# Kernel optimization log

Hardware: AMD Instinct MI355X
Metric: run time of the kernel (lower is better)

Reference implementation:

```python
import jax, jax.numpy as jnp
import numpy as np

B, J, C = 4096, 17, 512       # batch, joints (length), channels (dim)
K, TOK, CH, H, KS, G = 3, 64, 1024, 8, 3, 8  # adj kernels, tokens_dim, channels_dim, heads, conv_large, gn groups
EPS = 1e-5


def setup_inputs() -> dict:
    key = jax.random.key(0)
    ks = jax.random.split(key, 16)
    r = lambda i, shp, s=0.02: jax.random.normal(ks[i], shp, jnp.float32) * s
    return {
        "x": jax.random.normal(ks[0], (B, J, C), jnp.float32),
        "adj": jax.random.uniform(ks[1], (K, J, J), jnp.float32) / J,
        "norm1_w": jnp.ones((J,), jnp.float32), "norm1_b": jnp.zeros((J,), jnp.float32),
        "gcn1_w": r(2, (K * C, C)), "gcn1_b": jnp.zeros((K * C,), jnp.float32),
        "dw_w": r(3, (C, 1, KS), 0.1), "dw_b": jnp.zeros((C,), jnp.float32),
        "gn1_w": jnp.ones((C,), jnp.float32), "gn1_b": jnp.zeros((C,), jnp.float32),
        "pw_w": r(4, (C, C)), "pw_b": jnp.zeros((C,), jnp.float32),
        "mlp1_w1": r(5, (TOK, J)), "mlp1_b1": jnp.zeros((TOK,), jnp.float32),
        "mlp1_w2": r(6, (J, TOK)), "mlp1_b2": jnp.zeros((J,), jnp.float32),
        "qkv_w": r(7, (3 * C, C)), "qkv_b": jnp.zeros((3 * C,), jnp.float32),
        "proj_w": r(8, (C, C)), "proj_b": jnp.zeros((C,), jnp.float32),
        "gnf_w": jnp.ones((C,), jnp.float32), "gnf_b": jnp.zeros((C,), jnp.float32),
        "norm2_w": jnp.ones((C,), jnp.float32), "norm2_b": jnp.zeros((C,), jnp.float32),
        "mlp2_w1": r(9, (CH, C)), "mlp2_b1": jnp.zeros((CH,), jnp.float32),
        "mlp2_w2": r(10, (C, CH)), "mlp2_b2": jnp.zeros((C,), jnp.float32),
        "gcn2_w": r(11, (K * C, C)), "gcn2_b": jnp.zeros((K * C,), jnp.float32),
    }


def _gelu(t):
    return jax.nn.gelu(t, approximate=False)  # torch nn.GELU default is exact erf


def _ln(t, w, b):  # LayerNorm over last axis
    m = t.mean(-1, keepdims=True)
    v = ((t - m) ** 2).mean(-1, keepdims=True)
    return (t - m) * jax.lax.rsqrt(v + EPS) * w + b


def _gn(t, w, b):  # GroupNorm(G, C) over (B, C, J)
    Bn, Cc, Jn = t.shape
    r = t.reshape(Bn, G, -1)
    m = r.mean(-1, keepdims=True)
    v = ((r - m) ** 2).mean(-1, keepdims=True)
    r = (r - m) * jax.lax.rsqrt(v + EPS)
    return r.reshape(Bn, Cc, Jn) * w[:, None] + b[:, None]


def _gcn(t, w, b, adj):  # t: (B,C,J); 1x1 conv to K*C then einsum with adj (K,J,J)
    y = jnp.einsum('bcj,oc->boj', t, w) + b[:, None]
    y = y.reshape(t.shape[0], K, C, t.shape[2])
    return jnp.einsum('bkcv,kvw->bcw', y, adj)


def reference(x, adj, norm1_w, norm1_b, gcn1_w, gcn1_b, dw_w, dw_b, gn1_w, gn1_b,
              pw_w, pw_b, mlp1_w1, mlp1_b1, mlp1_w2, mlp1_b2, qkv_w, qkv_b,
              proj_w, proj_b, gnf_w, gnf_b, norm2_w, norm2_b,
              mlp2_w1, mlp2_b1, mlp2_w2, mlp2_b2, gcn2_w, gcn2_b):
    res = x                                   # (B,J,C)
    xc = jnp.swapaxes(x, 1, 2)                # (B,C,J)
    xc = _ln(xc, norm1_w, norm1_b)            # LayerNorm over joints

    # --- branch 1: GCN ---
    x_gcn1 = _gcn(xc, gcn1_w, gcn1_b, adj)    # (B,C,J)

    # --- branch 2: depthwise conv + token MLP ---
    h = jax.lax.conv_general_dilated(xc, dw_w, (1,), [(KS // 2, KS // 2)],
                                     dimension_numbers=('NCH', 'OIH', 'NCH'),
                                     feature_group_count=C) + dw_b[:, None]
    h = _gelu(_gn(h, gn1_w, gn1_b))
    h = jnp.einsum('bcj,oc->boj', h, pw_w) + pw_b[:, None]      # 1x1 conv
    h = _gelu(jnp.einsum('bcj,tj->bct', h, mlp1_w1) + mlp1_b1)  # token mlp fc1
    h = jnp.einsum('bct,jt->bcj', h, mlp1_w2) + mlp1_b2         # token mlp fc2

    # --- branch 3: global spatial attention over joints ---
    dh = C // H
    qkv = jnp.einsum('bcj,oc->boj', xc, qkv_w) + qkv_b[:, None]  # (B,3C,J)
    q, k_, v_ = jnp.split(qkv, 3, axis=1)
    q = q.reshape(-1, H, dh, J); k_ = k_.reshape(-1, H, dh, J); v_ = v_.reshape(-1, H, dh, J)
    attn = jax.nn.softmax(jnp.einsum('bhdi,bhdj->bhij', q, k_) / jnp.sqrt(jnp.float32(dh)), axis=-1)
    sga = jnp.einsum('bhij,bhdj->bhdi', attn, v_).reshape(-1, C, J)
    sga = jnp.einsum('bcj,oc->boj', sga, proj_w) + proj_b[:, None]

    # --- fuse ---
    xc = _gelu(_gn(sga + x_gcn1 + h, gnf_w, gnf_b))
    xj = jnp.swapaxes(xc, 1, 2)               # (B,J,C)
    res_channel = xj
    xn = _ln(xj + res, norm2_w, norm2_b)      # LayerNorm over channels
    m = _gelu(jnp.einsum('bjc,hc->bjh', xn, mlp2_w1) + mlp2_b1)
    m = jnp.einsum('bjh,ch->bjc', m, mlp2_w2) + mlp2_b2
    g2 = _gcn(jnp.swapaxes(m, 1, 2), gcn2_w, gcn2_b, adj)  # (B,C,J)
    xj = res_channel + jnp.swapaxes(g2, 1, 2)
    return xj + res
```

## Files before the change

kernel.cpp:

```cpp
#include <hip/hip_runtime.h>
#include <stdint.h>

#define BB 4096
#define JJ 17
#define CC 512

typedef unsigned short u16;
typedef __bf16 bf16x8 __attribute__((ext_vector_type(8)));
typedef float  f32x4  __attribute__((ext_vector_type(4)));

__device__ __forceinline__ float bf2f(u16 u){ return __uint_as_float(((uint32_t)u)<<16); }
__device__ __forceinline__ u16 f2bf(float f){
  uint32_t u = __float_as_uint(f);
  u += 0x7fffu + ((u>>16)&1u);
  return (u16)(u>>16);
}
__device__ __forceinline__ void unpk2(uint32_t u, float& lo, float& hi){
  lo = __uint_as_float(u<<16);
  hi = __uint_as_float(u & 0xffff0000u);
}
__device__ __forceinline__ float gelu_f(float x){
  float x2 = x*x;
  float y2 = x*fmaf(0.0713548162726f, x2, 1.59576912161f);
  float ey = __builtin_amdgcn_exp2f(y2*1.44269504089f);
  return fmaf(-x, __builtin_amdgcn_rcpf(ey+1.f), x);
}
__device__ __forceinline__ void gll16(const void* g, void* l){
  __builtin_amdgcn_global_load_lds(
      (const __attribute__((address_space(1))) void*)g,
      (__attribute__((address_space(3))) void*)l, 16, 0, 0);
}

__global__ void k_cvt7(const float* __restrict__ s0,const float* __restrict__ s1,
                       const float* __restrict__ s2,const float* __restrict__ s3,
                       const float* __restrict__ s4,const float* __restrict__ s5,
                       const float* __restrict__ s6, u16* __restrict__ out){
  int i = blockIdx.x*blockDim.x + threadIdx.x;
  if (i >= 3932160) return;
  const float* src; int off;
  if      (i < 786432)  { src=s0; off=0; }
  else if (i < 1572864) { src=s1; off=786432; }
  else if (i < 1835008) { src=s2; off=1572864; }
  else if (i < 2097152) { src=s3; off=1835008; }
  else if (i < 2621440) { src=s4; off=2097152; }
  else if (i < 3145728) { src=s5; off=2621440; }
  else                  { src=s6; off=3145728; }
  out[i] = f2bf(src[i-off]);
}

__global__ void k_tokprep(const float* __restrict__ w1, const float* __restrict__ w2,
                          u16* __restrict__ w1m, u16* __restrict__ w2m){
  int i = blockIdx.x*blockDim.x + threadIdx.x;
  if (i < 2560){ int t=i/40, j=i%40; w1m[i] = (j<17) ? f2bf(w1[t*17+j]) : (u16)0; }
  int k = i - 2560;
  if (k >= 0 && k < 2304){ int j=k/72, t=k%72; w2m[k] = (j<17 && t<64) ? f2bf(w2[j*64+t]) : (u16)0; }
}

__global__ __launch_bounds__(512) void k_pre(
    const float* __restrict__ x, int b0,
    const float* __restrict__ n1w, const float* __restrict__ n1b,
    const float* __restrict__ dww, const float* __restrict__ dwb,
    const float* __restrict__ gn1w, const float* __restrict__ gn1b,
    u16* __restrict__ xc, u16* __restrict__ hgn)
{
  int b = blockIdx.x, c = threadIdx.x;
  const float* xp = x + (size_t)(b0+b)*JJ*CC + c;
  float v[JJ]; float s = 0.f;
  #pragma unroll
  for (int j=0;j<JJ;j++){ v[j] = xp[(size_t)j*CC]; s += v[j]; }
  float mn = s*(1.f/JJ); float var = 0.f;
  #pragma unroll
  for (int j=0;j<JJ;j++){ float d=v[j]-mn; var += d*d; }
  float rr = rsqrtf(var*(1.f/JJ)+1e-5f);
  float xcv[JJ];
  #pragma unroll
  for (int j=0;j<JJ;j++) xcv[j] = (v[j]-mn)*rr*n1w[j] + n1b[j];
  u16* xo = xc + (size_t)b*JJ*CC + c;
  #pragma unroll
  for (int j=0;j<JJ;j++) xo[(size_t)j*CC] = f2bf(xcv[j]);
  float w0=dww[c*3+0], w1=dww[c*3+1], w2=dww[c*3+2], db=dwb[c];
  float h[JJ];
  #pragma unroll
  for (int j=0;j<JJ;j++){
    float a = db + w1*xcv[j];
    if (j>0)    a += w0*xcv[j-1];
    if (j<JJ-1) a += w2*xcv[j+1];
    h[j] = a;
  }
  float ss=0.f, sq=0.f;
  #pragma unroll
  for (int j=0;j<JJ;j++){ ss += h[j]; sq += h[j]*h[j]; }
  for (int off=32; off; off>>=1){ ss += __shfl_xor(ss,off); sq += __shfl_xor(sq,off); }
  float gm = ss*(1.f/(64.f*JJ));
  float gr = rsqrtf(sq*(1.f/(64.f*JJ)) - gm*gm + 1e-5f);
  float gw = gn1w[c], gb = gn1b[c];
  u16* ho = hgn + (size_t)b*JJ*CC + c;
  #pragma unroll
  for (int j=0;j<JJ;j++){
    float t = (h[j]-gm)*gr*gw + gb;
    ho[(size_t)j*CC] = f2bf(gelu_f(t));
  }
}

template<int DO_GELU, int DO_ADD>
__global__ __launch_bounds__(512,4) void gemm_r5(
    const u16* __restrict__ A, const u16* __restrict__ W, const float* __restrict__ bias,
    u16* __restrict__ out, const u16* __restrict__ add0, const u16* __restrict__ add1,
    int M, int N, int K, int NXT)
{
  __shared__ __align__(16) u16 lds[36864];
  const int tid = threadIdx.x;
  const int wid = tid>>6, lane = tid&63;

  const int nwg = gridDim.x;
  const int q8 = nwg>>3, r8 = nwg&7;
  const int xcd = blockIdx.x & 7, sub = blockIdx.x >> 3;
  const int wg = (xcd<r8 ? xcd*(q8+1) : r8*(q8+1)+(xcd-r8)*q8) + sub;
  const int n0 = (wg % NXT)*256;
  const int m0 = (wg / NXT)*128;

  const int wm = wid>>2, wn = wid&3;
  const int lr = lane&15, lg = lane>>4;
  const int T  = K>>5;

  const int agsw = ((tid&3) ^ ((tid>>3)&3))<<3;
  const u16* gA  = A + (size_t)(m0 + (tid>>2))*K + agsw;
  const u16* gB0 = W + (size_t)(n0 + (tid>>2))*K + agsw;
  const u16* gB1 = W + (size_t)(n0 + 128 + (tid>>2))*K + agsw;
  const int dstl = tid*8;

  const int g8 = (lg ^ ((lr>>1)&3))<<3;
  const int offA0 = (wm*64+lr)*32 + g8;
  const int offB0 = 4096 + (wn*64+lr)*32 + g8;

  f32x4 acc[4][4];
  #pragma unroll
  for (int i=0;i<4;i++)
    #pragma unroll
    for (int j=0;j<4;j++) acc[i][j] = (f32x4){0.f,0.f,0.f,0.f};

  auto STAGE = [&](int t, int sofs){
    gll16(gA  + t*32, lds + sofs + dstl);
    gll16(gB0 + t*32, lds + sofs + 4096 + dstl);
    gll16(gB1 + t*32, lds + sofs + 8192 + dstl);
  };

  STAGE(0, 0); STAGE(1, 12288);
  asm volatile("s_waitcnt vmcnt(3)" ::: "memory");
  __builtin_amdgcn_s_barrier();

  int s0 = 0, s1 = 12288, s2 = 24576;
  for (int t=0; t<T; ++t){
    const bool more = (t+2 < T);
    if (more) STAGE(t+2, s2);
    bf16x8 av[4], bv[4];
    #pragma unroll
    for (int i=0;i<4;i++) av[i] = *(const bf16x8*)&lds[s0 + offA0 + i*512];
    #pragma unroll
    for (int j=0;j<4;j++) bv[j] = *(const bf16x8*)&lds[s0 + offB0 + j*512];
    __builtin_amdgcn_s_setprio(1);
    #pragma unroll
    for (int i=0;i<4;i++)
      #pragma unroll
      for (int j=0;j<4;j++)
        acc[i][j] = __builtin_amdgcn_mfma_f32_16x16x32_bf16(av[i], bv[j], acc[i][j], 0,0,0);
    __builtin_amdgcn_s_setprio(0);
    if (more) asm volatile("s_waitcnt vmcnt(3)" ::: "memory");
    else      asm volatile("s_waitcnt vmcnt(0)" ::: "memory");
    __builtin_amdgcn_s_barrier();
    const int tmp = s0; s0 = s1; s1 = s2; s2 = tmp;
  }

  const int rbase = lg*4;
  #pragma unroll
  for (int i=0;i<4;i++){
    #pragma unroll
    for (int j=0;j<4;j++){
      const int col  = n0 + wn*64 + j*16 + lr;
      const int row0 = m0 + wm*64 + i*16 + rbase;
      const float bvl = bias[col];
      #pragma unroll
      for (int r=0;r<4;r++){
        size_t idx = (size_t)(row0+r)*N + col;
        float v = acc[i][j][r] + bvl;
        if (DO_ADD)  v += bf2f(add0[idx]) + bf2f(add1[idx]);
        if (DO_GELU) v = gelu_f(v);
        out[idx] = f2bf(v);
      }
    }
  }
}

template<int FINAL>
__global__ __launch_bounds__(512) void k_gcn2(
    const u16* __restrict__ G, const float* __restrict__ adj,
    u16* __restrict__ xg,
    const u16* __restrict__ tsum, int b0,
    float* __restrict__ out)
{
  __shared__ __align__(16) float adjp[51*20];
  const int tid = threadIdx.x;
  for (int i=tid; i<1020; i+=512){
    int r=i/20, cl=i%20;
    adjp[i] = (cl<17) ? adj[r*17+cl] : 0.f;
  }
  __syncthreads();

  const int sl  = tid>>7;
  const int l   = tid&127;
  const int c0  = l*4;
  const int bl  = blockIdx.x*4 + sl;

  float acc[JJ][4];
  #pragma unroll
  for (int w=0;w<JJ;w++)
    #pragma unroll
    for (int e=0;e<4;e++) acc[w][e]=0.f;

  const u16* gbase = G + (size_t)bl*JJ*1536 + c0;
  #pragma unroll 3
  for (int kv=0; kv<51; kv++){
    const int k = kv/JJ, v = kv - k*JJ;
    uint2 yu = *(const uint2*)(gbase + (size_t)v*1536 + k*512);
    float y0,y1,y2,y3;
    unpk2(yu.x, y0, y1);
    unpk2(yu.y, y2, y3);
    const f32x4* arow = (const f32x4*)&adjp[kv*20];
    f32x4 a0=arow[0], a1=arow[1], a2=arow[2], a3=arow[3];
    float a16 = adjp[kv*20+16];
    float ar[JJ] = {a0[0],a0[1],a0[2],a0[3], a1[0],a1[1],a1[2],a1[3],
                    a2[0],a2[1],a2[2],a2[3], a3[0],a3[1],a3[2],a3[3], a16};
    #pragma unroll
    for (int w=0;w<JJ;w++){
      acc[w][0] += y0*ar[w];
      acc[w][1] += y1*ar[w];
      acc[w][2] += y2*ar[w];
      acc[w][3] += y3*ar[w];
    }
  }

  if (FINAL==0){
    u16* xo = xg + (size_t)bl*JJ*CC + c0;
    #pragma unroll
    for (int w=0;w<JJ;w++){
      uint2 o;
      o.x = (uint32_t)f2bf(acc[w][0]) | ((uint32_t)f2bf(acc[w][1])<<16);
      o.y = (uint32_t)f2bf(acc[w][2]) | ((uint32_t)f2bf(acc[w][3])<<16);
      *(uint2*)(xo + (size_t)w*CC) = o;
    }
  } else {
    const size_t lb = (size_t)bl*JJ*CC + c0;
    const size_t gb = (size_t)(b0+bl)*JJ*CC + c0;
    #pragma unroll
    for (int w=0;w<JJ;w++){
      uint2 tu = *(const uint2*)(tsum + lb + (size_t)w*CC);
      float t0,t1,t2,t3;
      unpk2(tu.x, t0, t1);
      unpk2(tu.y, t2, t3);
      f32x4 o;
      o[0]=acc[w][0]+t0; o[1]=acc[w][1]+t1;
      o[2]=acc[w][2]+t2; o[3]=acc[w][3]+t3;
      *(f32x4*)(out + gb + (size_t)w*CC) = o;
    }
  }
}

__global__ __launch_bounds__(512) void k_attn(const u16* __restrict__ Gqkv, u16* __restrict__ sga){
  __shared__ __align__(16) u16 qs[8*17*72];
  __shared__ __align__(16) u16 ks_[8*17*72];
  __shared__ __align__(16) float at[8*17*20];
  int b = blockIdx.x, tid = threadIdx.x;
  int h = tid>>6, d = tid&63;
  const u16* base = Gqkv + (size_t)b*JJ*1536;
  float vv[JJ];
  #pragma unroll
  for (int i=0;i<JJ;i++){
    qs [(h*JJ+i)*72 + d] = base[(size_t)i*1536 +        h*64 + d];
    ks_[(h*JJ+i)*72 + d] = base[(size_t)i*1536 +  512 + h*64 + d];
    vv[i] = bf2f(base[(size_t)i*1536 + 1024 + h*64 + d]);
  }
  __syncthreads();
  for (int p=d; p<289; p+=64){
    int i=p/JJ, j=p-i*JJ;
    const u16* qrow = &qs [(h*JJ+i)*72];
    const u16* krow = &ks_[(h*JJ+j)*72];
    float a=0.f;
    #pragma unroll
    for (int t=0;t<8;t++){
      bf16x8 q8 = *(const bf16x8*)&qrow[t*8];
      bf16x8 k8 = *(const bf16x8*)&krow[t*8];
      #pragma unroll
      for (int e=0;e<8;e++) a += (float)q8[e]*(float)k8[e];
    }
    at[(h*JJ+i)*20 + j] = a*0.125f;
  }
  __syncthreads();
  if (d < JJ){
    float* row = &at[(h*JJ+d)*20];
    f32x4 r0=((f32x4*)row)[0], r1=((f32x4*)row)[1], r2=((f32x4*)row)[2], r3=((f32x4*)row)[3];
    float e16=row[16];
    float rv[JJ]={r0[0],r0[1],r0[2],r0[3],r1[0],r1[1],r1[2],r1[3],
                  r2[0],r2[1],r2[2],r2[3],r3[0],r3[1],r3[2],r3[3],e16};
    float mx=-1e30f;
    #pragma unroll
    for (int j=0;j<JJ;j++) mx=fmaxf(mx,rv[j]);
    float sm=0.f;
    #pragma unroll
    for (int j=0;j<JJ;j++){ rv[j]=__builtin_amdgcn_exp2f((rv[j]-mx)*1.44269504089f); sm+=rv[j]; }
    float inv=1.f/sm;
    #pragma unroll
    for (int j=0;j<JJ;j++) row[j]=rv[j]*inv;
  }
  __syncthreads();
  #pragma unroll
  for (int i=0;i<JJ;i++){
    const float* row = &at[(h*JJ+i)*20];
    f32x4 r0=((const f32x4*)row)[0], r1=((const f32x4*)row)[1],
          r2=((const f32x4*)row)[2], r3=((const f32x4*)row)[3];
    float a = r0[0]*vv[0]+r0[1]*vv[1]+r0[2]*vv[2]+r0[3]*vv[3]
            + r1[0]*vv[4]+r1[1]*vv[5]+r1[2]*vv[6]+r1[3]*vv[7]
            + r2[0]*vv[8]+r2[1]*vv[9]+r2[2]*vv[10]+r2[3]*vv[11]
            + r3[0]*vv[12]+r3[1]*vv[13]+r3[2]*vv[14]+r3[3]*vv[15]
            + row[16]*vv[16];
    sga[((size_t)b*JJ+i)*CC + h*64 + d] = f2bf(a);
  }
}

__global__ __launch_bounds__(256) void k_tok(const u16* __restrict__ Hpw,
    const u16* __restrict__ w1m, const u16* __restrict__ w2m,
    const float* __restrict__ b1, const float* __restrict__ b2,
    u16* __restrict__ h2o){
  __shared__ __align__(16) u16 lds[31488];
  __shared__ float b1s[64], b2s[32];
  const int tid = threadIdx.x, wid = tid>>6, lane = tid&63;
  const int lr = lane&15, lg = lane>>4;
  const int bl = blockIdx.x;
  const f32x4 zz = {0.f,0.f,0.f,0.f};

  for (int i=tid; i<2560; i+=256) lds[26624+i] = w1m[i];
  for (int i=tid; i<2304; i+=256) lds[29184+i] = w2m[i];
  if (tid<64) b1s[tid] = b1[tid];
  if (tid<32) b2s[tid] = (tid<17) ? b2[tid] : 0.f;
  {
    const int base = tid*40;
    lds[base+17]=0; lds[base+18]=0; lds[base+19]=0;
    #pragma unroll
    for (int q=0;q<5;q++) *(uint2*)&lds[base+20+q*4] = (uint2){0u,0u};
  }
  __syncthreads();

  const u16* hp = Hpw + (size_t)bl*JJ*CC;
  u16* op = h2o + (size_t)bl*JJ*CC;

  for (int pass=0; pass<2; ++pass){
    const int cbase = pass*256;
    for (int idx=tid; idx<1088; idx+=256){
      int j = idx>>6, cq = (idx&63)<<2;
      uint2 u = *(const uint2*)(hp + (size_t)j*CC + cbase + cq);
      lds[(cq  )*40 + j] = (u16)(u.x & 0xffffu);
      lds[(cq+1)*40 + j] = (u16)(u.x >> 16);
      lds[(cq+2)*40 + j] = (u16)(u.y & 0xffffu);
      lds[(cq+3)*40 + j] = (u16)(u.y >> 16);
    }
    __syncthreads();

    bf16x8 av1[4];
    #pragma unroll
    for (int mt=0;mt<4;mt++) av1[mt] = *(const bf16x8*)&lds[26624 + (mt*16+lr)*40 + lg*8];
    #pragma unroll
    for (int nt=0;nt<4;nt++){
      const int cl = wid*64 + nt*16 + lr;
      bf16x8 bv = *(const bf16x8*)&lds[cl*40 + lg*8];
      #pragma unroll
      for (int mt=0;mt<4;mt++){
        f32x4 ac = __builtin_amdgcn_mfma_f32_16x16x32_bf16(av1[mt], bv, zz, 0,0,0);
        const int t0 = mt*16 + lg*4;
        float g0 = gelu_f(ac[0] + b1s[t0+0]);
        float g1 = gelu_f(ac[1] + b1s[t0+1]);
        float g2 = gelu_f(ac[2] + b1s[t0+2]);
        float g3 = gelu_f(ac[3] + b1s[t0+3]);
        uint2 pk;
        pk.x = (uint32_t)f2bf(g0) | ((uint32_t)f2bf(g1)<<16);
        pk.y = (uint32_t)f2bf(g2) | ((uint32_t)f2bf(g3)<<16);
        const int gi = (10240 + cl*64 + t0) ^ ((cl&7)<<3);
        *(uint2*)&lds[gi] = pk;
      }
    }
    asm volatile("s_waitcnt lgkmcnt(0)" ::: "memory");
    __builtin_amdgcn_sched_barrier(0);

    bf16x8 av2[2][2];
    #pragma unroll
    for (int mt=0;mt<2;mt++)
      #pragma unroll
      for (int kt=0;kt<2;kt++)
        av2[mt][kt] = *(const bf16x8*)&lds[29184 + (mt*16+lr)*72 + kt*32 + lg*8];
    #pragma unroll
    for (int nt=0;nt<4;nt++){
      const int cl = wid*64 + nt*16 + lr;
      f32x4 a20 = zz, a21 = zz;
      #pragma unroll
      for (int kt=0;kt<2;kt++){
        const int gi = (10240 + cl*64 + kt*32 + lg*8) ^ ((cl&7)<<3);
        bf16x8 bv2 = *(const bf16x8*)&lds[gi];
        a20 = __builtin_amdgcn_mfma_f32_16x16x32_bf16(av2[0][kt], bv2, a20, 0,0,0);
        a21 = __builtin_amdgcn_mfma_f32_16x16x32_bf16(av2[1][kt], bv2, a21, 0,0,0);
      }
      const int c = cbase + cl;
      #pragma unroll
      for (int r=0;r<4;r++){
        const int j = lg*4 + r;
        op[(size_t)j*CC + c] = f2bf(a20[r] + b2s[j]);
      }
      if (lg==0) op[(size_t)16*CC + c] = f2bf(a21[0] + b2s[16]);
    }
    __syncthreads();
  }
}

__global__ __launch_bounds__(512) void k_fuse(const u16* __restrict__ s,
    const float* __restrict__ x, int b0,
    const float* __restrict__ gfw, const float* __restrict__ gfb,
    const float* __restrict__ n2w, const float* __restrict__ n2b,
    u16* __restrict__ tsum, u16* __restrict__ xn){
  __shared__ float rS[8][JJ], rQ[8][JJ];
  int b = blockIdx.x, c = threadIdx.x;
  int wave = c>>6, lane = c&63;
  const u16* sp = s + (size_t)b*JJ*CC + c;
  float sv[JJ];
  #pragma unroll
  for (int j=0;j<JJ;j++) sv[j]=bf2f(sp[(size_t)j*CC]);
  float ss=0.f, sq=0.f;
  #pragma unroll
  for (int j=0;j<JJ;j++){ ss+=sv[j]; sq+=sv[j]*sv[j]; }
  for (int off=32; off; off>>=1){ ss += __shfl_xor(ss,off); sq += __shfl_xor(sq,off); }
  float gm = ss*(1.f/1088.f);
  float gr = rsqrtf(sq*(1.f/1088.f) - gm*gm + 1e-5f);
  float gw=gfw[c], gb=gfb[c];
  const float* xp = x + (size_t)(b0+b)*JJ*CC + c;
  u16* tp = tsum + (size_t)b*JJ*CC + c;
  float t[JJ];
  #pragma unroll
  for (int j=0;j<JJ;j++){
    float v = gelu_f((sv[j]-gm)*gr*gw + gb);
    t[j] = v + xp[(size_t)j*CC];
    tp[(size_t)j*CC] = f2bf(t[j]);
  }
  #pragma unroll
  for (int j=0;j<JJ;j++){
    float a=t[j], q=a*a;
    for (int off=32; off; off>>=1){ a+=__shfl_xor(a,off); q+=__shfl_xor(q,off); }
    if (lane==0){ rS[wave][j]=a; rQ[wave][j]=q; }
  }
  __syncthreads();
  float wN=n2w[c], bN=n2b[c];
  u16* xo = xn + (size_t)b*JJ*CC + c;
  #pragma unroll
  for (int j=0;j<JJ;j++){
    float S=0.f,Q=0.f;
    #pragma unroll
    for (int w=0;w<8;w++){ S+=rS[w][j]; Q+=rQ[w][j]; }
    float mn=S*(1.f/512.f);
    float r2=rsqrtf(Q*(1.f/512.f)-mn*mn+1e-5f);
    xo[(size_t)j*CC]=f2bf((t[j]-mn)*r2*wN+bN);
  }
}

extern "C" void kernel_launch(void* const* d_in, const int* in_sizes, int n_in,
                              void* d_out, int out_size, void* d_ws, size_t ws_size,
                              hipStream_t stream)
{
  const float* x      = (const float*)d_in[0];
  const float* adj    = (const float*)d_in[1];
  const float* n1w    = (const float*)d_in[2];
  const float* n1b    = (const float*)d_in[3];
  const float* gcn1_w = (const float*)d_in[4];
  const float* gcn1_b = (const float*)d_in[5];
  const float* dw_w   = (const float*)d_in[6];
  const float* dw_b   = (const float*)d_in[7];
  const float* gn1_w  = (const float*)d_in[8];
  const float* gn1_b  = (const float*)d_in[9];
  const float* pw_w   = (const float*)d_in[10];
  const float* pw_b   = (const float*)d_in[11];
  const float* m1w1   = (const float*)d_in[12];
  const float* m1b1   = (const float*)d_in[13];
  const float* m1w2   = (const float*)d_in[14];
  const float* m1b2   = (const float*)d_in[15];
  const float* qkv_w  = (const float*)d_in[16];
  const float* qkv_b  = (const float*)d_in[17];
  const float* proj_w = (const float*)d_in[18];
  const float* proj_b = (const float*)d_in[19];
  const float* gnf_w  = (const float*)d_in[20];
  const float* gnf_b  = (const float*)d_in[21];
  const float* n2w    = (const float*)d_in[22];
  const float* n2b    = (const float*)d_in[23];
  const float* m2w1   = (const float*)d_in[24];
  const float* m2b1   = (const float*)d_in[25];
  const float* m2w2   = (const float*)d_in[26];
  const float* m2b2   = (const float*)d_in[27];
  const float* gcn2_w = (const float*)d_in[28];
  const float* gcn2_b = (const float*)d_in[29];
  float* out = (float*)d_out;

  char* ws = (char*)d_ws;
  const size_t WBYTES = (size_t)3932160*2;
  const size_t TPBYTES = (2560+2304)*2;

  const int cands[5] = {4096,2048,1024,512,256};
  int NB = 0;
  for (int ci=0; ci<5; ci++){
    size_t need = WBYTES + TPBYTES + (size_t)cands[ci]*JJ*2*(1536 + 4*512);
    if (need <= ws_size){ NB = cands[ci]; break; }
  }
  if (NB == 0) return;

  u16* wb = (u16*)ws;
  u16* w1m = (u16*)(ws + WBYTES);
  u16* w2m = w1m + 2560;
  char* p = ws + WBYTES + TPBYTES;
  const size_t SZ_BIGc = (size_t)NB*JJ*1536*2;
  const size_t SZTc    = (size_t)NB*JJ*512*2;
  u16* big = (u16*)p;               p += SZ_BIGc;
  u16* t0  = (u16*)p;               p += SZTc;
  u16* t1  = (u16*)p;               p += SZTc;
  u16* t2  = (u16*)p;               p += SZTc;
  u16* t3  = (u16*)p;

  u16 *wg1=wb, *wqkv=wb+786432, *wpw=wb+1572864, *wproj=wb+1835008,
      *wm1=wb+2097152, *wm2=wb+2621440, *wg2=wb+3145728;

  k_cvt7<<<(3932160+255)/256,256,0,stream>>>(gcn1_w,qkv_w,pw_w,proj_w,m2w1,m2w2,gcn2_w,wb);
  k_tokprep<<<19,256,0,stream>>>(m1w1,m1w2,w1m,w2m);

  const int M2 = NB*JJ;
  const int MT = M2/128;
  for (int b0 = 0; b0 < BB; b0 += NB){
    k_pre<<<NB,512,0,stream>>>(x,b0,n1w,n1b,dw_w,dw_b,gn1_w,gn1_b, t0, t1);
    gemm_r5<0,0><<<MT*6,512,0,stream>>>(t0,wg1,gcn1_b,big,nullptr,nullptr,M2,1536,512,6);
    k_gcn2<0><<<NB/4,512,0,stream>>>(big,adj,t2,nullptr,0,nullptr);
    gemm_r5<0,0><<<MT*6,512,0,stream>>>(t0,wqkv,qkv_b,big,nullptr,nullptr,M2,1536,512,6);
    k_attn<<<NB,512,0,stream>>>(big,t3);
    gemm_r5<0,0><<<MT*2,512,0,stream>>>(t1,wpw,pw_b,t0,nullptr,nullptr,M2,512,512,2);
    k_tok<<<NB,256,0,stream>>>(t0,w1m,w2m,m1b1,m1b2,t1);
    gemm_r5<0,1><<<MT*2,512,0,stream>>>(t3,wproj,proj_b,t0,t2,t1,M2,512,512,2);
    k_fuse<<<NB,512,0,stream>>>(t0,x,b0,gnf_w,gnf_b,n2w,n2b,t3,t2);
    gemm_r5<1,0><<<MT*4,512,0,stream>>>(t2,wm1,m2b1,big,nullptr,nullptr,M2,1024,512,4);
    gemm_r5<0,0><<<MT*2,512,0,stream>>>(big,wm2,m2b2,t0,nullptr,nullptr,M2,512,1024,2);
    gemm_r5<0,0><<<MT*6,512,0,stream>>>(t0,wg2,gcn2_b,big,nullptr,nullptr,M2,1536,512,6);
    k_gcn2<1><<<NB/4,512,0,stream>>>(big,adj,nullptr,t3,b0,out);
  }
}
```

Measured before the change: 1.329 ms.

## Enlarge GEMM tile to 256x256 with split-phase A/B staging

The shared bf16 GEMM used for all the linear layers now computes a 256x256 output tile per workgroup instead of 128x256. Each wave accumulates 8x4 MFMA tiles, and each K-step runs in two halves: the A loads for the next stage are issued before the first half and the B loads before the second, with an extra barrier in between. The aim is to reuse the B fragments across twice as many rows and to spread the global-to-LDS traffic across the iteration. The cost is more accumulator registers, a larger LDS buffer (occupancy drops to 2 workgroups), half as many workgroups in the grid, and a requirement that M be a multiple of 256.

```diff
diff --git a/kernel.cpp b/kernel.cpp
--- a/kernel.cpp
+++ b/kernel.cpp
@@ -103,12 +103,12 @@
 }
 
 template<int DO_GELU, int DO_ADD>
-__global__ __launch_bounds__(512,4) void gemm_r5(
+__global__ __launch_bounds__(512,2) void gemm_p2(
     const u16* __restrict__ A, const u16* __restrict__ W, const float* __restrict__ bias,
     u16* __restrict__ out, const u16* __restrict__ add0, const u16* __restrict__ add1,
     int M, int N, int K, int NXT)
 {
-  __shared__ __align__(16) u16 lds[36864];
+  __shared__ __align__(16) u16 lds[49152];
   const int tid = threadIdx.x;
   const int wid = tid>>6, lane = tid&63;
 
@@ -117,47 +117,51 @@
   const int xcd = blockIdx.x & 7, sub = blockIdx.x >> 3;
   const int wg = (xcd<r8 ? xcd*(q8+1) : r8*(q8+1)+(xcd-r8)*q8) + sub;
   const int n0 = (wg % NXT)*256;
-  const int m0 = (wg / NXT)*128;
+  const int m0 = (wg / NXT)*256;
 
   const int wm = wid>>2, wn = wid&3;
   const int lr = lane&15, lg = lane>>4;
   const int T  = K>>5;
 
-  const int agsw = ((tid&3) ^ ((tid>>3)&3))<<3;
-  const u16* gA  = A + (size_t)(m0 + (tid>>2))*K + agsw;
-  const u16* gB0 = W + (size_t)(n0 + (tid>>2))*K + agsw;
-  const u16* gB1 = W + (size_t)(n0 + 128 + (tid>>2))*K + agsw;
+  const int gswS = ((tid&3) ^ ((tid>>3)&3))<<3;
+  const u16* gA = A + (size_t)(m0 + (tid>>2))*K + gswS;
+  const u16* gB = W + (size_t)(n0 + (tid>>2))*K + gswS;
+  const int K128 = K<<7;
   const int dstl = tid*8;
 
   const int g8 = (lg ^ ((lr>>1)&3))<<3;
-  const int offA0 = (wm*64+lr)*32 + g8;
-  const int offB0 = 4096 + (wn*64+lr)*32 + g8;
-
-  f32x4 acc[4][4];
-  #pragma unroll
-  for (int i=0;i<4;i++)
+  const int offA = (wm*128+lr)*32 + g8;
+  const int offB = 8192 + (wn*64+lr)*32 + g8;
+
+  f32x4 acc[8][4];
+  #pragma unroll
+  for (int i=0;i<8;i++)
     #pragma unroll
     for (int j=0;j<4;j++) acc[i][j] = (f32x4){0.f,0.f,0.f,0.f};
 
-  auto STAGE = [&](int t, int sofs){
-    gll16(gA  + t*32, lds + sofs + dstl);
-    gll16(gB0 + t*32, lds + sofs + 4096 + dstl);
-    gll16(gB1 + t*32, lds + sofs + 8192 + dstl);
+  auto STAGE_A = [&](int t, int sofs){
+    gll16(gA + t*32,        lds + sofs + dstl);
+    gll16(gA + t*32 + K128, lds + sofs + 4096 + dstl);
   };
-
-  STAGE(0, 0); STAGE(1, 12288);
-  asm volatile("s_waitcnt vmcnt(3)" ::: "memory");
+  auto STAGE_B = [&](int t, int sofs){
+    gll16(gB + t*32,        lds + sofs + 8192 + dstl);
+    gll16(gB + t*32 + K128, lds + sofs + 12288 + dstl);
+  };
+
+  STAGE_A(0, 0); STAGE_B(0, 0);
+  STAGE_A(1, 16384); STAGE_B(1, 16384);
+  asm volatile("s_waitcnt vmcnt(4)" ::: "memory");
   __builtin_amdgcn_s_barrier();
 
-  int s0 = 0, s1 = 12288, s2 = 24576;
+  int s0 = 0, s1 = 16384, s2 = 32768;
   for (int t=0; t<T; ++t){
     const bool more = (t+2 < T);
-    if (more) STAGE(t+2, s2);
     bf16x8 av[4], bv[4];
-    #pragma unroll
-    for (int i=0;i<4;i++) av[i] = *(const bf16x8*)&lds[s0 + offA0 + i*512];
-    #pragma unroll
-    for (int j=0;j<4;j++) bv[j] = *(const bf16x8*)&lds[s0 + offB0 + j*512];
+    if (more) STAGE_A(t+2, s2);
+    #pragma unroll
+    for (int i=0;i<4;i++) av[i] = *(const bf16x8*)&lds[s0 + offA + i*512];
+    #pragma unroll
+    for (int j=0;j<4;j++) bv[j] = *(const bf16x8*)&lds[s0 + offB + j*512];
     __builtin_amdgcn_s_setprio(1);
     #pragma unroll
     for (int i=0;i<4;i++)
@@ -165,7 +169,18 @@
       for (int j=0;j<4;j++)
         acc[i][j] = __builtin_amdgcn_mfma_f32_16x16x32_bf16(av[i], bv[j], acc[i][j], 0,0,0);
     __builtin_amdgcn_s_setprio(0);
-    if (more) asm volatile("s_waitcnt vmcnt(3)" ::: "memory");
+    __builtin_amdgcn_s_barrier();
+    if (more) STAGE_B(t+2, s2);
+    #pragma unroll
+    for (int i=0;i<4;i++) av[i] = *(const bf16x8*)&lds[s0 + offA + 2048 + i*512];
+    __builtin_amdgcn_s_setprio(1);
+    #pragma unroll
+    for (int i=0;i<4;i++)
+      #pragma unroll
+      for (int j=0;j<4;j++)
+        acc[4+i][j] = __builtin_amdgcn_mfma_f32_16x16x32_bf16(av[i], bv[j], acc[4+i][j], 0,0,0);
+    __builtin_amdgcn_s_setprio(0);
+    if (more) asm volatile("s_waitcnt vmcnt(4)" ::: "memory");
     else      asm volatile("s_waitcnt vmcnt(0)" ::: "memory");
     __builtin_amdgcn_s_barrier();
     const int tmp = s0; s0 = s1; s1 = s2; s2 = tmp;
@@ -173,11 +188,11 @@
 
   const int rbase = lg*4;
   #pragma unroll
-  for (int i=0;i<4;i++){
+  for (int i=0;i<8;i++){
     #pragma unroll
     for (int j=0;j<4;j++){
       const int col  = n0 + wn*64 + j*16 + lr;
-      const int row0 = m0 + wm*64 + i*16 + rbase;
+      const int row0 = m0 + wm*128 + i*16 + rbase;
       const float bvl = bias[col];
       #pragma unroll
       for (int r=0;r<4;r++){
@@ -533,20 +548,20 @@
   k_tokprep<<<19,256,0,stream>>>(m1w1,m1w2,w1m,w2m);
 
   const int M2 = NB*JJ;
-  const int MT = M2/128;
+  const int MT = M2/256;
   for (int b0 = 0; b0 < BB; b0 += NB){
     k_pre<<<NB,512,0,stream>>>(x,b0,n1w,n1b,dw_w,dw_b,gn1_w,gn1_b, t0, t1);
-    gemm_r5<0,0><<<MT*6,512,0,stream>>>(t0,wg1,gcn1_b,big,nullptr,nullptr,M2,1536,512,6);
+    gemm_p2<0,0><<<MT*6,512,0,stream>>>(t0,wg1,gcn1_b,big,nullptr,nullptr,M2,1536,512,6);
     k_gcn2<0><<<NB/4,512,0,stream>>>(big,adj,t2,nullptr,0,nullptr);
-    gemm_r5<0,0><<<MT*6,512,0,stream>>>(t0,wqkv,qkv_b,big,nullptr,nullptr,M2,1536,512,6);
+    gemm_p2<0,0><<<MT*6,512,0,stream>>>(t0,wqkv,qkv_b,big,nullptr,nullptr,M2,1536,512,6);
     k_attn<<<NB,512,0,stream>>>(big,t3);
-    gemm_r5<0,0><<<MT*2,512,0,stream>>>(t1,wpw,pw_b,t0,nullptr,nullptr,M2,512,512,2);
+    gemm_p2<0,0><<<MT*2,512,0,stream>>>(t1,wpw,pw_b,t0,nullptr,nullptr,M2,512,512,2);
     k_tok<<<NB,256,0,stream>>>(t0,w1m,w2m,m1b1,m1b2,t1);
-    gemm_r5<0,1><<<MT*2,512,0,stream>>>(t3,wproj,proj_b,t0,t2,t1,M2,512,512,2);
+    gemm_p2<0,1><<<MT*2,512,0,stream>>>(t3,wproj,proj_b,t0,t2,t1,M2,512,512,2);
     k_fuse<<<NB,512,0,stream>>>(t0,x,b0,gnf_w,gnf_b,n2w,n2b,t3,t2);
-    gemm_r5<1,0><<<MT*4,512,0,stream>>>(t2,wm1,m2b1,big,nullptr,nullptr,M2,1024,512,4);
-    gemm_r5<0,0><<<MT*2,512,0,stream>>>(big,wm2,m2b2,t0,nullptr,nullptr,M2,512,1024,2);
-    gemm_r5<0,0><<<MT*6,512,0,stream>>>(t0,wg2,gcn2_b,big,nullptr,nullptr,M2,1536,512,6);
+    gemm_p2<1,0><<<MT*4,512,0,stream>>>(t2,wm1,m2b1,big,nullptr,nullptr,M2,1024,512,4);
+    gemm_p2<0,0><<<MT*2,512,0,stream>>>(big,wm2,m2b2,t0,nullptr,nullptr,M2,512,1024,2);
+    gemm_p2<0,0><<<MT*6,512,0,stream>>>(t0,wg2,gcn2_b,big,nullptr,nullptr,M2,1536,512,6);
     k_gcn2<1><<<NB/4,512,0,stream>>>(big,adj,nullptr,t3,b0,out);
   }
 }
```

After: 1.399 ms. 1.05x slower.

## Split fuse kernel into vectorized GroupNorm-GELU pass and per-token LayerNorm kernel

Applied to the files above, without the earlier changes.

The single fused GroupNorm+GELU+residual+LayerNorm kernel is split into two kernels. The first processes four batch items per block, with each thread handling four channels through packed 8-byte loads and stores. The second does a wave-per-token LayerNorm using 16-byte loads, which removes the shared-memory cross-wave reduction and barrier. The goal is wider coalesced memory access and fewer shuffles, at the cost of an extra launch and an extra read of the intermediate bf16 tensor.

```diff
diff --git a/kernel.cpp b/kernel.cpp
--- a/kernel.cpp
+++ b/kernel.cpp
@@ -418,52 +418,84 @@
   }
 }
 
-__global__ __launch_bounds__(512) void k_fuse(const u16* __restrict__ s,
+__global__ __launch_bounds__(512) void k_fuse_a(const u16* __restrict__ s,
     const float* __restrict__ x, int b0,
     const float* __restrict__ gfw, const float* __restrict__ gfb,
-    const float* __restrict__ n2w, const float* __restrict__ n2b,
-    u16* __restrict__ tsum, u16* __restrict__ xn){
-  __shared__ float rS[8][JJ], rQ[8][JJ];
-  int b = blockIdx.x, c = threadIdx.x;
-  int wave = c>>6, lane = c&63;
-  const u16* sp = s + (size_t)b*JJ*CC + c;
-  float sv[JJ];
-  #pragma unroll
-  for (int j=0;j<JJ;j++) sv[j]=bf2f(sp[(size_t)j*CC]);
+    u16* __restrict__ tsum){
+  const int tid = threadIdx.x;
+  const int sl  = tid>>7;
+  const int l   = tid&127;
+  const int c0  = l*4;
+  const int bl  = blockIdx.x*4 + sl;
+
+  const u16* sp = s + (size_t)bl*JJ*CC + c0;
+  float sv[JJ][4];
   float ss=0.f, sq=0.f;
   #pragma unroll
-  for (int j=0;j<JJ;j++){ ss+=sv[j]; sq+=sv[j]*sv[j]; }
-  for (int off=32; off; off>>=1){ ss += __shfl_xor(ss,off); sq += __shfl_xor(sq,off); }
+  for (int j=0;j<JJ;j++){
+    uint2 u = *(const uint2*)(sp + (size_t)j*CC);
+    unpk2(u.x, sv[j][0], sv[j][1]);
+    unpk2(u.y, sv[j][2], sv[j][3]);
+    #pragma unroll
+    for (int e=0;e<4;e++){ ss += sv[j][e]; sq = fmaf(sv[j][e], sv[j][e], sq); }
+  }
+  #pragma unroll
+  for (int off=8; off; off>>=1){ ss += __shfl_xor(ss,off); sq += __shfl_xor(sq,off); }
   float gm = ss*(1.f/1088.f);
   float gr = rsqrtf(sq*(1.f/1088.f) - gm*gm + 1e-5f);
-  float gw=gfw[c], gb=gfb[c];
-  const float* xp = x + (size_t)(b0+b)*JJ*CC + c;
-  u16* tp = tsum + (size_t)b*JJ*CC + c;
-  float t[JJ];
+
+  f32x4 gw = *(const f32x4*)(gfw + c0);
+  f32x4 gb = *(const f32x4*)(gfb + c0);
+  const float* xp = x + (size_t)(b0+bl)*JJ*CC + c0;
+  u16* tp = tsum + (size_t)bl*JJ*CC + c0;
   #pragma unroll
   for (int j=0;j<JJ;j++){
-    float v = gelu_f((sv[j]-gm)*gr*gw + gb);
-    t[j] = v + xp[(size_t)j*CC];
-    tp[(size_t)j*CC] = f2bf(t[j]);
-  }
-  #pragma unroll
-  for (int j=0;j<JJ;j++){
-    float a=t[j], q=a*a;
-    for (int off=32; off; off>>=1){ a+=__shfl_xor(a,off); q+=__shfl_xor(q,off); }
-    if (lane==0){ rS[wave][j]=a; rQ[wave][j]=q; }
-  }
-  __syncthreads();
-  float wN=n2w[c], bN=n2b[c];
-  u16* xo = xn + (size_t)b*JJ*CC + c;
-  #pragma unroll
-  for (int j=0;j<JJ;j++){
-    float S=0.f,Q=0.f;
-    #pragma unroll
-    for (int w=0;w<8;w++){ S+=rS[w][j]; Q+=rQ[w][j]; }
-    float mn=S*(1.f/512.f);
-    float r2=rsqrtf(Q*(1.f/512.f)-mn*mn+1e-5f);
-    xo[(size_t)j*CC]=f2bf((t[j]-mn)*r2*wN+bN);
-  }
+    f32x4 xv = *(const f32x4*)(xp + (size_t)j*CC);
+    float t0 = gelu_f((sv[j][0]-gm)*gr*gw[0] + gb[0]) + xv[0];
+    float t1 = gelu_f((sv[j][1]-gm)*gr*gw[1] + gb[1]) + xv[1];
+    float t2 = gelu_f((sv[j][2]-gm)*gr*gw[2] + gb[2]) + xv[2];
+    float t3 = gelu_f((sv[j][3]-gm)*gr*gw[3] + gb[3]) + xv[3];
+    uint2 o;
+    o.x = (uint32_t)f2bf(t0) | ((uint32_t)f2bf(t1)<<16);
+    o.y = (uint32_t)f2bf(t2) | ((uint32_t)f2bf(t3)<<16);
+    *(uint2*)(tp + (size_t)j*CC) = o;
+  }
+}
+
+__global__ __launch_bounds__(512) void k_ln(const u16* __restrict__ tsum,
+    const float* __restrict__ n2w, const float* __restrict__ n2b,
+    u16* __restrict__ xn){
+  const int wid = threadIdx.x>>6, lane = threadIdx.x&63;
+  const size_t tk = (size_t)blockIdx.x*8 + wid;
+  const u16* tp = tsum + tk*CC + lane*8;
+  uint4 u = *(const uint4*)tp;
+  float v[8];
+  unpk2(u.x, v[0], v[1]);
+  unpk2(u.y, v[2], v[3]);
+  unpk2(u.z, v[4], v[5]);
+  unpk2(u.w, v[6], v[7]);
+  float ss=0.f, sq=0.f;
+  #pragma unroll
+  for (int e=0;e<8;e++){ ss += v[e]; sq = fmaf(v[e], v[e], sq); }
+  #pragma unroll
+  for (int off=32; off; off>>=1){ ss += __shfl_xor(ss,off); sq += __shfl_xor(sq,off); }
+  float mn = ss*(1.f/512.f);
+  float r2 = rsqrtf(sq*(1.f/512.f) - mn*mn + 1e-5f);
+  f32x4 w0 = *(const f32x4*)(n2w + lane*8);
+  f32x4 w1 = *(const f32x4*)(n2w + lane*8 + 4);
+  f32x4 b0 = *(const f32x4*)(n2b + lane*8);
+  f32x4 b1 = *(const f32x4*)(n2b + lane*8 + 4);
+  float wv[8] = {w0[0],w0[1],w0[2],w0[3], w1[0],w1[1],w1[2],w1[3]};
+  float bv[8] = {b0[0],b0[1],b0[2],b0[3], b1[0],b1[1],b1[2],b1[3]};
+  u16 o[8];
+  #pragma unroll
+  for (int e=0;e<8;e++) o[e] = f2bf((v[e]-mn)*r2*wv[e] + bv[e]);
+  uint4 pk;
+  pk.x = (uint32_t)o[0] | ((uint32_t)o[1]<<16);
+  pk.y = (uint32_t)o[2] | ((uint32_t)o[3]<<16);
+  pk.z = (uint32_t)o[4] | ((uint32_t)o[5]<<16);
+  pk.w = (uint32_t)o[6] | ((uint32_t)o[7]<<16);
+  *(uint4*)(xn + tk*CC + lane*8) = pk;
 }
 
 extern "C" void kernel_launch(void* const* d_in, const int* in_sizes, int n_in,
@@ -543,7 +575,8 @@
     gemm_r5<0,0><<<MT*2,512,0,stream>>>(t1,wpw,pw_b,t0,nullptr,nullptr,M2,512,512,2);
     k_tok<<<NB,256,0,stream>>>(t0,w1m,w2m,m1b1,m1b2,t1);
     gemm_r5<0,1><<<MT*2,512,0,stream>>>(t3,wproj,proj_b,t0,t2,t1,M2,512,512,2);
-    k_fuse<<<NB,512,0,stream>>>(t0,x,b0,gnf_w,gnf_b,n2w,n2b,t3,t2);
+    k_fuse_a<<<NB/4,512,0,stream>>>(t0,x,b0,gnf_w,gnf_b,t3);
+    k_ln<<<M2/8,512,0,stream>>>(t3,n2w,n2b,t2);
     gemm_r5<1,0><<<MT*4,512,0,stream>>>(t2,wm1,m2b1,big,nullptr,nullptr,M2,1024,512,4);
     gemm_r5<0,0><<<MT*2,512,0,stream>>>(big,wm2,m2b2,t0,nullptr,nullptr,M2,512,1024,2);
     gemm_r5<0,0><<<MT*6,512,0,stream>>>(t0,wg2,gcn2_b,big,nullptr,nullptr,M2,1536,512,6);
```

Measured after the change: 1.259 ms (median of 2 runs). -5.2%, faster.
